# Kernel tuning notes

Hardware: AMD Instinct MI355X
Metric: run time of the kernel (lower is better)

The kernel has to match this reference:

```python
import jax, jax.numpy as jnp
import numpy as np
from jax.ops import segment_sum, segment_max

NEG_SLOPE = 0.2  # PyG GATv2Conv default

def _gatv2(x, ei, ea, Wl, bl, Wr, br, We, att, b, n):
    # PyG GATv2Conv, heads=1, concat=True, add_self_loops=True, fill_value='mean'
    src, dst = ei[0], ei[1]
    ones = jnp.ones((src.shape[0],), x.dtype)
    deg = segment_sum(ones, dst, num_segments=n)
    ea_mean = segment_sum(ea, dst, num_segments=n) / jnp.maximum(deg, 1.0)[:, None]
    loop = jnp.arange(n, dtype=src.dtype)
    src = jnp.concatenate([src, loop]); dst = jnp.concatenate([dst, loop])
    ea = jnp.concatenate([ea, ea_mean], axis=0)
    xl = x @ Wl.T + bl          # lin_l, used for both message and source term
    xr = x @ Wr.T + br          # lin_r, target term
    h = jax.nn.leaky_relu(xl[src] + xr[dst] + ea @ We.T, NEG_SLOPE)  # [E+N, F]
    logits = h @ att            # [E+N]
    m = segment_max(logits, dst, num_segments=n)   # every node has a self-loop -> finite
    p = jnp.exp(logits - m[dst])
    denom = segment_sum(p, dst, num_segments=n)
    alpha = p / denom[dst]
    return segment_sum(alpha[:, None] * xl[src], dst, num_segments=n) + b

def _mean_pool(h, seg, num):
    s = segment_sum(h, seg, num_segments=num)
    c = segment_sum(jnp.ones(h.shape[:1], h.dtype), seg, num_segments=num)
    return s / jnp.maximum(c, 1.0)[:, None]

def setup_inputs() -> dict:
    key = jax.random.key(0)
    ks = iter(jax.random.split(key, 64))
    def nrm(shape, scale=None):
        s = scale if scale is not None else 1.0 / np.sqrt(shape[-1])
        return jax.random.normal(next(ks), shape, jnp.float32) * s
    N, E = 80000, 1280000
    NR, ER, R = 20480, 40960, 512
    inp = {
        'x': nrm((N, 16), 1.0),
        'edge_attr': nrm((E, 18), 1.0),
        'rule_x': nrm((NR, 16), 1.0),
        'rule_edge_attr': nrm((ER, 18), 1.0),
    }
    def gat(fi, fo):
        return (nrm((fo, fi)), jnp.zeros(fo), nrm((fo, fi)), jnp.zeros(fo),
                nrm((fo, 18)), nrm((fo,), 1.0 / np.sqrt(fo)), jnp.zeros(fo))
    for name, (fi, fo) in [('gat0', (16, 100)), ('gat1', (16, 100)), ('gat2', (100, 200))]:
        for suf, v in zip(['Wl', 'bl', 'Wr', 'br', 'We', 'att', 'b'], gat(fi, fo)):
            inp[name + '_' + suf] = v
    inp['lin_W'] = nrm((400, 200)); inp['lin_b'] = jnp.zeros(400)
    inp['f1_W'] = nrm((200, 400)); inp['f1_b'] = jnp.zeros(200)
    inp['f2_W'] = nrm((100, 200)); inp['f2_b'] = jnp.zeros(100)
    inp['f3_W'] = nrm((100, 100)); inp['f3_b'] = jnp.zeros(100)
    inp['bil_W'] = nrm((1, 100, 100)); inp['bil_b'] = jnp.zeros(1)
    inp['edge_index'] = jax.random.randint(next(ks), (2, E), 0, N, dtype=jnp.int32)
    inp['batch'] = jnp.zeros((N,), jnp.int32)
    inp['rule_edge_index'] = jax.random.randint(next(ks), (2, ER), 0, NR, dtype=jnp.int32)
    inp['rule_batch'] = jnp.sort(jax.random.randint(next(ks), (NR,), 0, R, dtype=jnp.int32))
    inp['n_rules'] = R
    return inp

def reference(x, edge_attr, rule_x, rule_edge_attr,
              gat0_Wl, gat0_bl, gat0_Wr, gat0_br, gat0_We, gat0_att, gat0_b,
              gat1_Wl, gat1_bl, gat1_Wr, gat1_br, gat1_We, gat1_att, gat1_b,
              gat2_Wl, gat2_bl, gat2_Wr, gat2_br, gat2_We, gat2_att, gat2_b,
              lin_W, lin_b, f1_W, f1_b, f2_W, f2_b, f3_W, f3_b, bil_W, bil_b,
              edge_index, batch, rule_edge_index, rule_batch, n_rules):
    N = x.shape[0]; NR = rule_x.shape[0]
    # --- RuleParse path ---
    h = jax.nn.relu(_gatv2(rule_x, rule_edge_index, rule_edge_attr,
                           gat1_Wl, gat1_bl, gat1_Wr, gat1_br, gat1_We, gat1_att, gat1_b, NR))
    h = jax.nn.relu(_gatv2(h, rule_edge_index, rule_edge_attr,
                           gat2_Wl, gat2_bl, gat2_Wr, gat2_br, gat2_We, gat2_att, gat2_b, NR))
    h = h @ lin_W.T + lin_b                          # [NR, 400]
    y = _mean_pool(h, rule_batch, n_rules)           # [R, 400]
    y = jax.nn.relu(y @ f1_W.T + f1_b)
    y = jax.nn.relu(y @ f2_W.T + f2_b)
    y = y @ f3_W.T + f3_b                            # [R, 100]
    # --- data path ---
    g = _gatv2(x, edge_index, edge_attr,
               gat0_Wl, gat0_bl, gat0_Wr, gat0_br, gat0_We, gat0_att, gat0_b, N)
    xp = _mean_pool(g, batch, 1)                     # single graph -> [1, 100]
    xr = jnp.tile(xp, (n_rules, 1))                  # x.repeat(len(rules), 1)
    out = jnp.einsum('nd,ode,ne->no', xr, bil_W, y) + bil_b  # Bilinear(100,100,1) -> [R,1]
    return out.T.squeeze()                           # [R]
```

## Files before the change

### kernel.cpp

```cpp
#include <hip/hip_runtime.h>

#define NS 0.2f

__global__ void k_deg(const int* __restrict__ dst, int* degi, int E){
  int stride = gridDim.x * blockDim.x;
  for(int e = blockIdx.x * blockDim.x + threadIdx.x; e < E; e += stride)
    atomicAdd(&degi[dst[e]], 1);
}

__device__ __forceinline__ int wave_iscan(int v, int lane){
  #pragma unroll
  for(int o = 1; o < 64; o <<= 1){
    int t = __shfl_up(v, o);
    if(lane >= o) v += t;
  }
  return v;
}

__global__ __launch_bounds__(1024) void k_scan_sum(
    const int* __restrict__ deg, int* __restrict__ bsum, int n)
{
  __shared__ int wsum[16];
  const int lane = threadIdx.x & 63;
  const int w = threadIdx.x >> 6;
  int idx = blockIdx.x * 1024 + threadIdx.x;
  int v = (idx < n) ? deg[idx] : 0;
  #pragma unroll
  for(int o = 32; o; o >>= 1) v += __shfl_xor(v, o);
  if(lane == 0) wsum[w] = v;
  __syncthreads();
  if(w == 0){
    int s = (lane < 16) ? wsum[lane] : 0;
    #pragma unroll
// ... 22 lines not shown
    const int* __restrict__ deg, const int* __restrict__ bsum,
    int* __restrict__ rowoff, int* __restrict__ pos, int n)
{
  __shared__ int wsum[16];
  const int lane = threadIdx.x & 63;
  const int w = threadIdx.x >> 6;
  int idx = blockIdx.x * 1024 + threadIdx.x;
  int v = (idx < n) ? deg[idx] : 0;
  int inc = wave_iscan(v, lane);
  if(lane == 63) wsum[w] = inc;
  __syncthreads();
  if(w == 0){
    int s = (lane < 16) ? wsum[lane] : 0;
    s = wave_iscan(s, lane);
    if(lane < 16) wsum[lane] = s;
  }
  __syncthreads();
  int woff = (w > 0) ? wsum[w - 1] : 0;
  if(idx < n){
    int ex = bsum[blockIdx.x] + woff + inc - v;
    rowoff[idx] = ex;
    pos[idx] = ex;
  }
}

__global__ void k_fill(const int* __restrict__ dst, int* pos, int* eidx, int E){
  int stride = gridDim.x * blockDim.x;
  for(int e = blockIdx.x * blockDim.x + threadIdx.x; e < E; e += stride){
    int slot = atomicAdd(&pos[dst[e]], 1);
    eidx[slot] = e;
  }
}

__global__ __launch_bounds__(256) void k_easum(
    const float* __restrict__ ea, const int* __restrict__ rowoff,
    const int* __restrict__ eidx, float* __restrict__ eam, int n)
{
  const int lane = threadIdx.x & 63;
  const int wid  = threadIdx.x >> 6;
  const int i = blockIdx.x * 4 + wid;
  if(i >= n) return;
  const int r0 = rowoff[i], r1 = rowoff[i + 1];
  const int deg = r1 - r0;
  const int pg = lane / 18;
  const int k  = lane - pg * 18;
  float s = 0.0f;
  if(pg < 3){
    for(int p = r0 + pg; p < r1; p += 3)
      s += ea[(long)eidx[p] * 18 + k];
  }
  float b = __shfl(s, lane + 18);
  float c = __shfl(s, lane + 36);
  if(lane < 18) eam[(long)i * 18 + lane] = (s + b + c) / fmaxf((float)deg, 1.0f);
}

#define BM 64
#define BN 64
#define BK 16
__global__ __launch_bounds__(256) void k_gemm(
    const float* __restrict__ A, const float* __restrict__ W,
    const float* __restrict__ b, float* __restrict__ C,
    int n, int K, int M, int dorelu)
{
  __shared__ float As[BK][BM + 4];
  __shared__ float Bs[BK][BN + 4];
  const int bi = blockIdx.x * BM;
  const int bj = blockIdx.y * BN;
  const int tid = threadIdx.x;
  const int tr = tid / 16, tc = tid % 16;
  float acc[4][4] = {};
  for(int k0 = 0; k0 < K; k0 += BK){
    for(int l = tid; l < BM * BK; l += 256){
      int c = l % BK, r = l / BK;
      int gr = bi + r, gc = k0 + c;
      As[c][r] = (gr < n && gc < K) ? A[(long)gr * K + gc] : 0.0f;
    }
    for(int l = tid; l < BN * BK; l += 256){
      int c = l % BK, r = l / BK;
      int gr = bj + r, gc = k0 + c;
      Bs[c][r] = (gr < M && gc < K) ? W[(long)gr * K + gc] : 0.0f;
    }
    __syncthreads();
    #pragma unroll
    for(int kk = 0; kk < BK; ++kk){
      float4 av = *(const float4*)&As[kk][tr * 4];
      float4 bv = *(const float4*)&Bs[kk][tc * 4];
      acc[0][0] = fmaf(av.x, bv.x, acc[0][0]); acc[0][1] = fmaf(av.x, bv.y, acc[0][1]);
      acc[0][2] = fmaf(av.x, bv.z, acc[0][2]); acc[0][3] = fmaf(av.x, bv.w, acc[0][3]);
      acc[1][0] = fmaf(av.y, bv.x, acc[1][0]); acc[1][1] = fmaf(av.y, bv.y, acc[1][1]);
      acc[1][2] = fmaf(av.y, bv.z, acc[1][2]); acc[1][3] = fmaf(av.y, bv.w, acc[1][3]);
      acc[2][0] = fmaf(av.z, bv.x, acc[2][0]); acc[2][1] = fmaf(av.z, bv.y, acc[2][1]);
      acc[2][2] = fmaf(av.z, bv.z, acc[2][2]); acc[2][3] = fmaf(av.z, bv.w, acc[2][3]);
      acc[3][0] = fmaf(av.w, bv.x, acc[3][0]); acc[3][1] = fmaf(av.w, bv.y, acc[3][1]);
      acc[3][2] = fmaf(av.w, bv.z, acc[3][2]); acc[3][3] = fmaf(av.w, bv.w, acc[3][3]);
    }
    __syncthreads();
  }
  for(int r = 0; r < 4; r++){
    int gr = bi + tr * 4 + r;
    if(gr >= n) continue;
    for(int c = 0; c < 4; c++){
      int gc = bj + tc * 4 + c;
      if(gc >= M) continue;
      float val = acc[r][c] + b[gc];
      C[(long)gr * M + gc] = dorelu ? fmaxf(val, 0.0f) : val;
    }
  }
}

static void gemm_launch(const float* A, const float* W, const float* b, float* C,
                        int n, int K, int M, int relu, hipStream_t s){
  dim3 grid((n + BM - 1) / BM, (M + BN - 1) / BN);
  k_gemm<<<grid, 256, 0, s>>>(A, W, b, C, n, K, M, relu);
}

__device__ __forceinline__ float lkrelu(float t){ return (t > 0.0f) ? t : NS * t; }

template<int G, int F>
__global__ __launch_bounds__(256) void k_edge_logits(
    const float* __restrict__ xl, const float* __restrict__ xr,
    const float* __restrict__ ea,
    const int* __restrict__ src, const int* __restrict__ dst,
    const int* __restrict__ eidx,
    const float* __restrict__ We, const float* __restrict__ att,
    float2* __restrict__ lw, int E)
{
  constexpr int NG = 256 / G;
  constexpr int NE = 4;
  constexpr int FQ = F / 4;
  __shared__ float4 sWeT[18 * FQ];
  __shared__ float4 sAtt[FQ];
  __shared__ float4 sEa[NG][18];
  __shared__ int    sIdx[NG][3][NE];

  const int tid = threadIdx.x;
  for(int idx = tid; idx < F * 18; idx += 256){
    int f = idx / 18, k = idx % 18;
    ((float*)sWeT)[k * F + f] = We[idx];
  }
  for(int f = tid; f < F; f += 256) ((float*)sAtt)[f] = att[f];
  __syncthreads();

  const int g  = tid / G;
  const int gl = tid % G;
  const bool act = (gl * 4 < F);
  const int glc = act ? gl : 0;
  const long step = (long)gridDim.x * (NG * NE);

  for(long base = (long)blockIdx.x * (NG * NE); base < (long)E; base += step){
    const long pb = base + (long)g * NE;
    if(gl < NE){
      long p = pb + gl;
      int e = -1, s = 0, d = 0;
      if(p < (long)E){ e = eidx[p]; s = src[e]; d = dst[e]; }
      sIdx[g][0][gl] = e; sIdx[g][1][gl] = s; sIdx[g][2][gl] = d;
    }
    #pragma unroll
    for(int t = 0; t < (9 * NE + G - 1) / G; ++t){
      int u = t * G + gl;
      if(u < 9 * NE){
        int ne = u & 3, k2 = u >> 2;
        int e = sIdx[g][0][ne];
        float2 v = (e >= 0) ? *(const float2*)(ea + (long)e * 18 + k2 * 2)
                            : make_float2(0.0f, 0.0f);
        ((float*)&sEa[g][k2 * 2 + 0])[ne] = v.x;
        ((float*)&sEa[g][k2 * 2 + 1])[ne] = v.y;
      }
    }
    int4 sv = *(const int4*)&sIdx[g][1][0];
    int4 dv = *(const int4*)&sIdx[g][2][0];
    float4 a0 = *(const float4*)(xl + (long)sv.x * F + glc * 4);
    float4 b0 = *(const float4*)(xr + (long)dv.x * F + glc * 4);
    float4 a1 = *(const float4*)(xl + (long)sv.y * F + glc * 4);
    float4 b1 = *(const float4*)(xr + (long)dv.y * F + glc * 4);
    float4 a2 = *(const float4*)(xl + (long)sv.z * F + glc * 4);
    float4 b2 = *(const float4*)(xr + (long)dv.z * F + glc * 4);
    float4 a3 = *(const float4*)(xl + (long)sv.w * F + glc * 4);
    float4 b3 = *(const float4*)(xr + (long)dv.w * F + glc * 4);
    float4 t0 = make_float4(a0.x + b0.x, a0.y + b0.y, a0.z + b0.z, a0.w + b0.w);
    float4 t1 = make_float4(a1.x + b1.x, a1.y + b1.y, a1.z + b1.z, a1.w + b1.w);
    float4 t2 = make_float4(a2.x + b2.x, a2.y + b2.y, a2.z + b2.z, a2.w + b2.w);
    float4 t3 = make_float4(a3.x + b3.x, a3.y + b3.y, a3.z + b3.z, a3.w + b3.w);
    #pragma unroll
    for(int k = 0; k < 18; ++k){
      float4 w  = sWeT[k * FQ + glc];
      float4 eq = sEa[g][k];
      t0.x = fmaf(w.x, eq.x, t0.x); t0.y = fmaf(w.y, eq.x, t0.y);
      t0.z = fmaf(w.z, eq.x, t0.z); t0.w = fmaf(w.w, eq.x, t0.w);
      t1.x = fmaf(w.x, eq.y, t1.x); t1.y = fmaf(w.y, eq.y, t1.y);
      t1.z = fmaf(w.z, eq.y, t1.z); t1.w = fmaf(w.w, eq.y, t1.w);
      t2.x = fmaf(w.x, eq.z, t2.x); t2.y = fmaf(w.y, eq.z, t2.y);
      t2.z = fmaf(w.z, eq.z, t2.z); t2.w = fmaf(w.w, eq.z, t2.w);
      t3.x = fmaf(w.x, eq.w, t3.x); t3.y = fmaf(w.y, eq.w, t3.y);
      t3.z = fmaf(w.z, eq.w, t3.z); t3.w = fmaf(w.w, eq.w, t3.w);
    }
    float4 av = sAtt[glc];
    float r0 = 0, r1 = 0, r2 = 0, r3 = 0;
    if(act){
      r0 = av.x * lkrelu(t0.x) + av.y * lkrelu(t0.y) + av.z * lkrelu(t0.z) + av.w * lkrelu(t0.w);
      r1 = av.x * lkrelu(t1.x) + av.y * lkrelu(t1.y) + av.z * lkrelu(t1.z) + av.w * lkrelu(t1.w);
      r2 = av.x * lkrelu(t2.x) + av.y * lkrelu(t2.y) + av.z * lkrelu(t2.z) + av.w * lkrelu(t2.w);
      r3 = av.x * lkrelu(t3.x) + av.y * lkrelu(t3.y) + av.z * lkrelu(t3.z) + av.w * lkrelu(t3.w);
    }
    #pragma unroll
    for(int o = G / 2; o; o >>= 1){
      r0 += __shfl_xor(r0, o);
      r1 += __shfl_xor(r1, o);
      r2 += __shfl_xor(r2, o);
      r3 += __shfl_xor(r3, o);
    }
    if(gl == 0 && pb + 0 < (long)E) lw[pb + 0] = make_float2(r0, __int_as_float(sv.x));
    if(gl == 1 && pb + 1 < (long)E) lw[pb + 1] = make_float2(r1, __int_as_float(sv.y));
    if(gl == 2 && pb + 2 < (long)E) lw[pb + 2] = make_float2(r2, __int_as_float(sv.z));
    if(gl == 3 && pb + 3 < (long)E) lw[pb + 3] = make_float2(r3, __int_as_float(sv.w));
  }
}

#define CH 128
template<int JMAX>
__global__ __launch_bounds__(256) void k_gat_agg(
    const float* __restrict__ xl, const float* __restrict__ xr,
    const float* __restrict__ eam,
    const float* __restrict__ We, const float* __restrict__ att,
    const int* __restrict__ rowoff, const float2* __restrict__ lw,
    const float* __restrict__ bias, float* __restrict__ out,
    int n, int F, int dorelu)
{
  const int lane = threadIdx.x & 63;
  const int wid  = threadIdx.x >> 6;
  __shared__ float2 s_ws[4][CH];
  const int i = blockIdx.x * 4 + wid;
  if(i >= n) return;
  const int r0 = rowoff[i], r1 = rowoff[i + 1];
  const int deg = r1 - r0;

  float eamv[18];
  #pragma unroll
  for(int k = 0; k < 18; ++k) eamv[k] = eam[(long)i * 18 + k];

  float selfl = 0.0f;
  float acc[JMAX];
  #pragma unroll
  for(int j = 0; j < JMAX; ++j){
    int f = lane + j * 64;
    float xv = (f < F) ? xl[(long)i * F + f] : 0.0f;
    acc[j] = xv;
    if(f < F){
      float t = xv + xr[(long)i * F + f];
      const float* w = We + f * 18;
      #pragma unroll
      for(int k = 0; k < 18; ++k) t = fmaf(w[k], eamv[k], t);
      t = lkrelu(t);
      selfl = fmaf(att[f], t, selfl);
    }
  }
  #pragma unroll
  for(int o = 32; o; o >>= 1) selfl += __shfl_xor(selfl, o);

  float m = selfl, denom = 1.0f;

  for(int c0 = 0; c0 < deg; c0 += CH){
    int cn = min(CH, deg - c0);
    float lmax = -3.4e38f;
    for(int q = lane; q < cn; q += 64){
      float2 ws = lw[r0 + c0 + q];
      s_ws[wid][q] = ws;
      lmax = fmaxf(lmax, ws.x);
    }
    #pragma unroll
    for(int o = 32; o; o >>= 1) lmax = fmaxf(lmax, __shfl_xor(lmax, o));
    float newm = fmaxf(m, lmax);
    float scale = __expf(m - newm);
    denom *= scale;
    #pragma unroll
    for(int j = 0; j < JMAX; ++j) acc[j] *= scale;
    m = newm;
    float psum = 0.0f;
    for(int q = lane; q < cn; q += 64){
      float2 ws = s_ws[wid][q];
      float w = __expf(ws.x - m);
      s_ws[wid][q].x = w;
      psum += w;
    }
    #pragma unroll
    for(int o = 32; o; o >>= 1) psum += __shfl_xor(psum, o);
    denom += psum;
    int p = 0;
    for(; p + 8 <= cn; p += 8){
      float2 wv[8];
      const float* xs[8];
      #pragma unroll
      for(int u = 0; u < 8; ++u){
        wv[u] = s_ws[wid][p + u];
        xs[u] = xl + (long)__float_as_int(wv[u].y) * F;
      }
      float vv[8][JMAX];
      #pragma unroll
      for(int u = 0; u < 8; ++u)
        #pragma unroll
        for(int j = 0; j < JMAX; ++j){
          int f = lane + j * 64;
          vv[u][j] = (f < F) ? xs[u][f] : 0.0f;
        }
      #pragma unroll
      for(int u = 0; u < 8; ++u)
        #pragma unroll
        for(int j = 0; j < JMAX; ++j)
          acc[j] = fmaf(wv[u].x, vv[u][j], acc[j]);
    }
    for(; p < cn; ++p){
      float2 ws = s_ws[wid][p];
      const float* xs = xl + (long)__float_as_int(ws.y) * F;
      #pragma unroll
      for(int j = 0; j < JMAX; ++j){
        int f = lane + j * 64;
        if(f < F) acc[j] = fmaf(ws.x, xs[f], acc[j]);
      }
    }
  }

  float inv = 1.0f / denom;
  #pragma unroll
  for(int j = 0; j < JMAX; ++j){
    int f = lane + j * 64;
    if(f < F){
      float o = acc[j] * inv + bias[f];
      out[(long)i * F + f] = dorelu ? fmaxf(o, 0.0f) : o;
    }
  }
}

__global__ void k_rule_starts(const int* __restrict__ rb, int* starts, int NR, int R){
  int r = blockIdx.x * blockDim.x + threadIdx.x;
  if(r > R) return;
  if(r == R){ starts[R] = NR; return; }
  int lo = 0, hi = NR;
  while(lo < hi){ int mid = (lo + hi) >> 1; if(rb[mid] < r) lo = mid + 1; else hi = mid; }
  starts[r] = lo;
}

__global__ void k_pool_rules(const float* __restrict__ h, const int* __restrict__ starts,
                             float* __restrict__ y, int R, int F){
  long idx = (long)blockIdx.x * blockDim.x + threadIdx.x;
  long total = (long)R * F;
  if(idx >= total) return;
  int r = (int)(idx / F);
  int f = (int)(idx % F);
  int s0 = starts[r], s1 = starts[r + 1];
  float a = 0.0f;
  for(int i = s0; i < s1; i++) a += h[(long)i * F + f];
  y[idx] = a / fmaxf((float)(s1 - s0), 1.0f);
}

__global__ __launch_bounds__(256) void k_pool_all(
    const float* __restrict__ g, float* xp, int n, int F)
{
  const int lane = threadIdx.x & 63;
  const int wid  = threadIdx.x >> 6;
  const int nw   = 4;
  float a0 = 0.0f, a1 = 0.0f;
// ... 15 lines not shown
  }
}

__global__ __launch_bounds__(512) void k_bil(
    const float* __restrict__ xp, const float* __restrict__ Wb,
    const float* __restrict__ y, const float* __restrict__ bilb,
    float* __restrict__ out, float inv_n, int R)
{
  __shared__ float v[100];
  int t = threadIdx.x;
  if(t < 100){
    float a = 0.0f;
    for(int d = 0; d < 100; d++) a += xp[d] * Wb[d * 100 + t];
    v[t] = a * inv_n;
  }
  __syncthreads();
  for(int r = t; r < R; r += 512){
    float a = 0.0f;
    const float* yr = y + (long)r * 100;
    for(int e = 0; e < 100; e++) a += v[e] * yr[e];
    out[r] = a + bilb[0];
  }
}

static inline int nblk(long n){
  long b = (n + 255) / 256;
  if(b > 20480) b = 20480;
  if(b < 1) b = 1;
  return (int)b;
}

struct GatParams { const float *Wl,*bl,*Wr,*br,*We,*att,*b; };

template<int G, int F>
static void logits_launch(const float* xl, const float* xr, const float* ea,
                          const int* src, const int* dst, const int* eidx,
                          const float* We, const float* att, float2* lw,
                          int E, hipStream_t stream){
  const int epb = (256 / G) * 4;
  long nb = ((long)E + epb - 1) / epb;
  int grid = (int)(nb < 2048 ? nb : 2048);
  k_edge_logits<G, F><<<grid, 256, 0, stream>>>(xl, xr, ea, src, dst, eidx, We, att, lw, E);
}

static void scan_launch(const int* degi, int* bsum, int* rowoff, int* pos,
                        int n, hipStream_t stream){
  int B = (n + 1023) / 1024;
  k_scan_sum  <<<B, 1024, 0, stream>>>(degi, bsum, n);
  k_scan_bsum <<<1, 128,  0, stream>>>(bsum, rowoff, B, n);
  k_scan_apply<<<B, 1024, 0, stream>>>(degi, bsum, rowoff, pos, n);
}

static void run_gatv2(const float* x, int fin, int fout, int n,
                      const int* src, const int* dst, const float* ea, int E,
                      GatParams P, float* out, int dorelu,
                      float* xl, float* xr, float2* lw,
                      const float* eam, const int* rowoff, const int* eidx,
                      hipStream_t stream){
  gemm_launch(x, P.Wl, P.bl, xl, n, fin, fout, 0, stream);
  gemm_launch(x, P.Wr, P.br, xr, n, fin, fout, 0, stream);
  if(fout == 100){
    logits_launch<32, 100>(xl, xr, ea, src, dst, eidx, P.We, P.att, lw, E, stream);
    k_gat_agg<2><<<(n + 3) / 4, 256, 0, stream>>>(xl, xr, eam, P.We, P.att,
                                                  rowoff, lw, P.b, out, n, fout, dorelu);
  } else {
    logits_launch<64, 200>(xl, xr, ea, src, dst, eidx, P.We, P.att, lw, E, stream);
    k_gat_agg<4><<<(n + 3) / 4, 256, 0, stream>>>(xl, xr, eam, P.We, P.att,
                                                  rowoff, lw, P.b, out, n, fout, dorelu);
  }
}

extern "C" void kernel_launch(void* const* d_in, const int* in_sizes, int n_in,
                              void* d_out, int out_size, void* d_ws, size_t ws_size,
                              hipStream_t stream){
  const float* x   = (const float*)d_in[0];
  const float* ea  = (const float*)d_in[1];
  const float* rx  = (const float*)d_in[2];
  const float* rea = (const float*)d_in[3];
  GatParams g0{ (const float*)d_in[4],  (const float*)d_in[5],  (const float*)d_in[6],
                (const float*)d_in[7],  (const float*)d_in[8],  (const float*)d_in[9],
                (const float*)d_in[10] };
  GatParams g1{ (const float*)d_in[11], (const float*)d_in[12], (const float*)d_in[13],
                (const float*)d_in[14], (const float*)d_in[15], (const float*)d_in[16],
                (const float*)d_in[17] };
  GatParams g2{ (const float*)d_in[18], (const float*)d_in[19], (const float*)d_in[20],
                (const float*)d_in[21], (const float*)d_in[22], (const float*)d_in[23],
                (const float*)d_in[24] };
  const float* lin_W = (const float*)d_in[25]; const float* lin_b = (const float*)d_in[26];
  const float* f1_W  = (const float*)d_in[27]; const float* f1_b  = (const float*)d_in[28];
  const float* f2_W  = (const float*)d_in[29]; const float* f2_b  = (const float*)d_in[30];
  const float* f3_W  = (const float*)d_in[31]; const float* f3_b  = (const float*)d_in[32];
  const float* bilW  = (const float*)d_in[33]; const float* bilb  = (const float*)d_in[34];
  const int* ei  = (const int*)d_in[35];
  const int* rei = (const int*)d_in[37];
  const int* rb  = (const int*)d_in[38];

  const int N  = in_sizes[0] / 16;
  const int E  = in_sizes[1] / 18;
  const int NR = in_sizes[2] / 16;
  const int ER = in_sizes[3] / 18;
  const int R  = out_size;

  float* Wf = (float*)d_ws;
  size_t off = 0;
  auto alloc  = [&](size_t nf){ nf = (nf + 1) & ~(size_t)1; float* p = Wf + off; off += nf; return p; };
  auto alloci = [&](size_t ni){ ni = (ni + 1) & ~(size_t)1; int* p = (int*)(Wf + off); off += ni; return p; };

  float* y0 = alloc((size_t)R * 400);
  float* y1 = alloc((size_t)R * 200);
  float* y2 = alloc((size_t)R * 100);
  float* y3 = alloc((size_t)R * 100);
  float* xp = alloc(128);
  int* starts = alloci(R + 1);
  const size_t arena = off;

  {
    off = arena;
    float* h1 = alloc((size_t)NR * 100);
    float* h2 = alloc((size_t)NR * 200);
    float* xl = alloc((size_t)NR * 200);
    float* xr = alloc((size_t)NR * 200);
    float2* lw = (float2*)alloc((size_t)ER * 2);
    float* eam   = alloc((size_t)NR * 18);
    int* rowoff = alloci(NR + 1);
    int* degi   = alloci(NR);
    int* pos    = alloci(NR);
    int* bsum   = alloci(128);
    int* eidx   = alloci(ER);
    const int* rsrc = rei; const int* rdst = rei + ER;

    hipMemsetAsync(degi, 0, (size_t)NR * 4, stream);
    k_deg<<<nblk(ER), 256, 0, stream>>>(rdst, degi, ER);
    scan_launch(degi, bsum, rowoff, pos, NR, stream);
    k_fill<<<nblk(ER), 256, 0, stream>>>(rdst, pos, eidx, ER);
    k_easum<<<(NR + 3) / 4, 256, 0, stream>>>(rea, rowoff, eidx, eam, NR);

    run_gatv2(rx, 16, 100, NR, rsrc, rdst, rea, ER, g1, h1, 1,
              xl, xr, lw, eam, rowoff, eidx, stream);
    run_gatv2(h1, 100, 200, NR, rsrc, rdst, rea, ER, g2, h2, 1,
              xl, xr, lw, eam, rowoff, eidx, stream);

    float* hlin = xl;
    gemm_launch(h2, lin_W, lin_b, hlin, NR, 200, 400, 0, stream);

    k_rule_starts<<<(R + 256) / 256, 256, 0, stream>>>(rb, starts, NR, R);
    k_pool_rules<<<nblk((long)R * 400), 256, 0, stream>>>(hlin, starts, y0, R, 400);

    gemm_launch(y0, f1_W, f1_b, y1, R, 400, 200, 1, stream);
    gemm_launch(y1, f2_W, f2_b, y2, R, 200, 100, 1, stream);
    gemm_launch(y2, f3_W, f3_b, y3, R, 100, 100, 0, stream);
  }

  {
    off = arena;
    float* g  = alloc((size_t)N * 100);
    float* xl = alloc((size_t)N * 100);
    float* xr = alloc((size_t)N * 100);
    float2* lw = (float2*)alloc((size_t)E * 2);
    float* eam   = alloc((size_t)N * 18);
    int* rowoff = alloci((size_t)N + 1);
    int* degi   = alloci(N);
    int* pos    = alloci(N);
    int* bsum   = alloci(128);
    int* eidx   = alloci(E);
    const int* srcp = ei; const int* dstp = ei + E;

    hipMemsetAsync(degi, 0, (size_t)N * 4, stream);
    k_deg<<<nblk(E), 256, 0, stream>>>(dstp, degi, E);
    scan_launch(degi, bsum, rowoff, pos, N, stream);
    k_fill<<<nblk(E), 256, 0, stream>>>(dstp, pos, eidx, E);
    k_easum<<<(N + 3) / 4, 256, 0, stream>>>(ea, rowoff, eidx, eam, N);

    run_gatv2(x, 16, 100, N, srcp, dstp, ea, E, g0, g, 0,
              xl, xr, lw, eam, rowoff, eidx, stream);

    hipMemsetAsync(xp, 0, 128 * 4, stream);
    k_pool_all<<<1024, 256, 0, stream>>>(g, xp, N, 100);
    k_bil<<<1, 512, 0, stream>>>(xp, bilW, y3, bilb, (float*)d_out, 1.0f / (float)N, R);
  }
}
```

Baseline: 1.032 ms.

## Fuse GATv2 edge logits, self-loop mean, and aggregation into one CSR kernel; fp16 xl/xr

Replaces the separate edge-logit kernel, edge-attr mean kernel and aggregation kernel with one node-centric kernel. It walks each destination's CSR edge list, computes logits, runs an online softmax and accumulates messages in a single pass. The mean edge attribute is built on the fly for the self-loop term. For the large data graph, the xl/xr projections are stored in fp16 to halve gather traffic. This removes the intermediate logit buffer and extra passes, at the cost of fp16 rounding and possible load imbalance on high-degree nodes.

```diff
diff --git a/kernel.cpp b/kernel.cpp
--- a/kernel.cpp
+++ b/kernel.cpp
@@ -1,4 +1,5 @@
 #include <hip/hip_runtime.h>
+#include <hip/hip_fp16.h>
 
 #define NS 0.2f
 
@@ -87,28 +88,6 @@
   }
 }
 
-__global__ __launch_bounds__(256) void k_easum(
-    const float* __restrict__ ea, const int* __restrict__ rowoff,
-    const int* __restrict__ eidx, float* __restrict__ eam, int n)
-{
-  const int lane = threadIdx.x & 63;
-  const int wid  = threadIdx.x >> 6;
-  const int i = blockIdx.x * 4 + wid;
-  if(i >= n) return;
-  const int r0 = rowoff[i], r1 = rowoff[i + 1];
-  const int deg = r1 - r0;
-  const int pg = lane / 18;
-  const int k  = lane - pg * 18;
-  float s = 0.0f;
-  if(pg < 3){
-    for(int p = r0 + pg; p < r1; p += 3)
-      s += ea[(long)eidx[p] * 18 + k];
-  }
-  float b = __shfl(s, lane + 18);
-  float c = __shfl(s, lane + 36);
-  if(lane < 18) eam[(long)i * 18 + lane] = (s + b + c) / fmaxf((float)deg, 1.0f);
-}
-
 #define BM 64
 #define BN 64
 #define BK 16
@@ -163,30 +142,98 @@
   }
 }
 
+__global__ __launch_bounds__(256) void k_gemm_h(
+    const float* __restrict__ A, const float* __restrict__ W,
+    const float* __restrict__ b, __half* __restrict__ C,
+    int n, int K, int M)
+{
+  __shared__ float As[BK][BM + 4];
+  __shared__ float Bs[BK][BN + 4];
+  const int bi = blockIdx.x * BM;
+  const int bj = blockIdx.y * BN;
+  const int tid = threadIdx.x;
+  const int tr = tid / 16, tc = tid % 16;
+  float acc[4][4] = {};
+  for(int k0 = 0; k0 < K; k0 += BK){
+    for(int l = tid; l < BM * BK; l += 256){
+      int c = l % BK, r = l / BK;
+      int gr = bi + r, gc = k0 + c;
+      As[c][r] = (gr < n && gc < K) ? A[(long)gr * K + gc] : 0.0f;
+    }
+    for(int l = tid; l < BN * BK; l += 256){
+      int c = l % BK, r = l / BK;
+      int gr = bj + r, gc = k0 + c;
+      Bs[c][r] = (gr < M && gc < K) ? W[(long)gr * K + gc] : 0.0f;
+    }
+    __syncthreads();
+    #pragma unroll
+    for(int kk = 0; kk < BK; ++kk){
+      float4 av = *(const float4*)&As[kk][tr * 4];
+      float4 bv = *(const float4*)&Bs[kk][tc * 4];
+      acc[0][0] = fmaf(av.x, bv.x, acc[0][0]); acc[0][1] = fmaf(av.x, bv.y, acc[0][1]);
+      acc[0][2] = fmaf(av.x, bv.z, acc[0][2]); acc[0][3] = fmaf(av.x, bv.w, acc[0][3]);
+      acc[1][0] = fmaf(av.y, bv.x, acc[1][0]); acc[1][1] = fmaf(av.y, bv.y, acc[1][1]);
+      acc[1][2] = fmaf(av.y, bv.z, acc[1][2]); acc[1][3] = fmaf(av.y, bv.w, acc[1][3]);
+      acc[2][0] = fmaf(av.z, bv.x, acc[2][0]); acc[2][1] = fmaf(av.z, bv.y, acc[2][1]);
+      acc[2][2] = fmaf(av.z, bv.z, acc[2][2]); acc[2][3] = fmaf(av.z, bv.w, acc[2][3]);
+      acc[3][0] = fmaf(av.w, bv.x, acc[3][0]); acc[3][1] = fmaf(av.w, bv.y, acc[3][1]);
+      acc[3][2] = fmaf(av.w, bv.z, acc[3][2]); acc[3][3] = fmaf(av.w, bv.w, acc[3][3]);
+    }
+    __syncthreads();
+  }
+  for(int r = 0; r < 4; r++){
+    int gr = bi + tr * 4 + r;
+    if(gr >= n) continue;
+    int gc0 = bj + tc * 4;
+    float v[4];
+    #pragma unroll
+    for(int c = 0; c < 4; c++){
+      int gc = gc0 + c;
+      v[c] = (gc < M) ? acc[r][c] + b[gc] : 0.0f;
+    }
+    __half* Crow = C + (long)gr * M;
+    if(gc0 + 3 < M){
+      *(__half2*)(Crow + gc0)     = __halves2half2(__float2half(v[0]), __float2half(v[1]));
+      *(__half2*)(Crow + gc0 + 2) = __halves2half2(__float2half(v[2]), __float2half(v[3]));
+    } else {
+      for(int c = 0; c < 4; c++){
+        int gc = gc0 + c;
+        if(gc < M) Crow[gc] = __float2half(v[c]);
+      }
+    }
+  }
+}
+
 static void gemm_launch(const float* A, const float* W, const float* b, float* C,
                         int n, int K, int M, int relu, hipStream_t s){
   dim3 grid((n + BM - 1) / BM, (M + BN - 1) / BN);
   k_gemm<<<grid, 256, 0, s>>>(A, W, b, C, n, K, M, relu);
 }
 
+static void gemm_h_launch(const float* A, const float* W, const float* b, __half* C,
+                          int n, int K, int M, hipStream_t s){
+  dim3 grid((n + BM - 1) / BM, (M + BN - 1) / BN);
+  k_gemm_h<<<grid, 256, 0, s>>>(A, W, b, C, n, K, M);
+}
+
 __device__ __forceinline__ float lkrelu(float t){ return (t > 0.0f) ? t : NS * t; }
 
 template<int G, int F>
-__global__ __launch_bounds__(256) void k_edge_logits(
+__global__ __launch_bounds__(256) void k_gat_fused(
     const float* __restrict__ xl, const float* __restrict__ xr,
-    const float* __restrict__ ea,
-    const int* __restrict__ src, const int* __restrict__ dst,
-    const int* __restrict__ eidx,
+    const float* __restrict__ ea, const int* __restrict__ src,
+    const int* __restrict__ rowoff, const int* __restrict__ eidx,
     const float* __restrict__ We, const float* __restrict__ att,
-    float2* __restrict__ lw, int E)
+    const float* __restrict__ bias, float* __restrict__ out,
+    int n, int dorelu)
 {
   constexpr int NG = 256 / G;
-  constexpr int NE = 4;
   constexpr int FQ = F / 4;
   __shared__ float4 sWeT[18 * FQ];
   __shared__ float4 sAtt[FQ];
   __shared__ float4 sEa[NG][18];
-  __shared__ int    sIdx[NG][3][NE];
+  __shared__ float  sEamAcc[NG][18];
+  __shared__ int    sIdx[NG][2][4];
 
   const int tid = threadIdx.x;
   for(int idx = tid; idx < F * 18; idx += 256){
@@ -196,191 +243,279 @@
   for(int f = tid; f < F; f += 256) ((float*)sAtt)[f] = att[f];
   __syncthreads();
 
-  const int g  = tid / G;
-  const int gl = tid % G;
+  const int g = tid / G, gl = tid % G;
   const bool act = (gl * 4 < F);
   const int glc = act ? gl : 0;
-  const long step = (long)gridDim.x * (NG * NE);
-
-  for(long base = (long)blockIdx.x * (NG * NE); base < (long)E; base += step){
-    const long pb = base + (long)g * NE;
-    if(gl < NE){
-      long p = pb + gl;
-      int e = -1, s = 0, d = 0;
-      if(p < (long)E){ e = eidx[p]; s = src[e]; d = dst[e]; }
-      sIdx[g][0][gl] = e; sIdx[g][1][gl] = s; sIdx[g][2][gl] = d;
-    }
-    #pragma unroll
-    for(int t = 0; t < (9 * NE + G - 1) / G; ++t){
-      int u = t * G + gl;
-      if(u < 9 * NE){
-        int ne = u & 3, k2 = u >> 2;
-        int e = sIdx[g][0][ne];
-        float2 v = (e >= 0) ? *(const float2*)(ea + (long)e * 18 + k2 * 2)
-                            : make_float2(0.0f, 0.0f);
-        ((float*)&sEa[g][k2 * 2 + 0])[ne] = v.x;
-        ((float*)&sEa[g][k2 * 2 + 1])[ne] = v.y;
-      }
-    }
-    int4 sv = *(const int4*)&sIdx[g][1][0];
-    int4 dv = *(const int4*)&sIdx[g][2][0];
-    float4 a0 = *(const float4*)(xl + (long)sv.x * F + glc * 4);
-    float4 b0 = *(const float4*)(xr + (long)dv.x * F + glc * 4);
-    float4 a1 = *(const float4*)(xl + (long)sv.y * F + glc * 4);
-    float4 b1 = *(const float4*)(xr + (long)dv.y * F + glc * 4);
-    float4 a2 = *(const float4*)(xl + (long)sv.z * F + glc * 4);
-    float4 b2 = *(const float4*)(xr + (long)dv.z * F + glc * 4);
-    float4 a3 = *(const float4*)(xl + (long)sv.w * F + glc * 4);
-    float4 b3 = *(const float4*)(xr + (long)dv.w * F + glc * 4);
-    float4 t0 = make_float4(a0.x + b0.x, a0.y + b0.y, a0.z + b0.z, a0.w + b0.w);
-    float4 t1 = make_float4(a1.x + b1.x, a1.y + b1.y, a1.z + b1.z, a1.w + b1.w);
-    float4 t2 = make_float4(a2.x + b2.x, a2.y + b2.y, a2.z + b2.z, a2.w + b2.w);
-    float4 t3 = make_float4(a3.x + b3.x, a3.y + b3.y, a3.z + b3.z, a3.w + b3.w);
+  const float4 av = sAtt[glc];
+
+  for(int node = blockIdx.x * NG + g; node < n; node += gridDim.x * NG){
+    const int r0 = rowoff[node], r1 = rowoff[node + 1];
+    const int deg = r1 - r0;
+    if(gl < 18) sEamAcc[g][gl] = 0.0f;
+    float4 xlv = *(const float4*)(xl + (long)node * F + glc * 4);
+    float4 xrv = *(const float4*)(xr + (long)node * F + glc * 4);
+    float m = -3.4e38f, denom = 0.0f;
+    float4 acc = make_float4(0.f, 0.f, 0.f, 0.f);
+
+    for(int p = r0; p < r1; p += 4){
+      if(gl < 4){
+        int pp = p + gl; int e = -1, s = 0;
+        if(pp < r1){ e = eidx[pp]; s = src[e]; }
+        sIdx[g][0][gl] = e; sIdx[g][1][gl] = s;
+      }
+      #pragma unroll
+      for(int t = 0; t < (36 + G - 1) / G; ++t){
+        int u = t * G + gl;
+        if(u < 36){
+          int ne = u & 3, k2 = u >> 2;
+          int e = sIdx[g][0][ne];
+          float2 v = (e >= 0) ? *(const float2*)(ea + (long)e * 18 + k2 * 2)
+                              : make_float2(0.f, 0.f);
+          ((float*)&sEa[g][k2 * 2 + 0])[ne] = v.x;
+          ((float*)&sEa[g][k2 * 2 + 1])[ne] = v.y;
+        }
+      }
+      int4 sv = *(const int4*)&sIdx[g][1][0];
+      if(gl < 18){ float4 eq = sEa[g][gl]; sEamAcc[g][gl] += eq.x + eq.y + eq.z + eq.w; }
+      float4 a0 = *(const float4*)(xl + (long)sv.x * F + glc * 4);
+      float4 a1 = *(const float4*)(xl + (long)sv.y * F + glc * 4);
+      float4 a2 = *(const float4*)(xl + (long)sv.z * F + glc * 4);
+      float4 a3 = *(const float4*)(xl + (long)sv.w * F + glc * 4);
+      float4 t0 = make_float4(a0.x + xrv.x, a0.y + xrv.y, a0.z + xrv.z, a0.w + xrv.w);
+      float4 t1 = make_float4(a1.x + xrv.x, a1.y + xrv.y, a1.z + xrv.z, a1.w + xrv.w);
+      float4 t2 = make_float4(a2.x + xrv.x, a2.y + xrv.y, a2.z + xrv.z, a2.w + xrv.w);
+      float4 t3 = make_float4(a3.x + xrv.x, a3.y + xrv.y, a3.z + xrv.z, a3.w + xrv.w);
+      #pragma unroll
+      for(int k = 0; k < 18; ++k){
+        float4 w  = sWeT[k * FQ + glc];
+        float4 eq = sEa[g][k];
+        t0.x = fmaf(w.x, eq.x, t0.x); t0.y = fmaf(w.y, eq.x, t0.y);
+        t0.z = fmaf(w.z, eq.x, t0.z); t0.w = fmaf(w.w, eq.x, t0.w);
+        t1.x = fmaf(w.x, eq.y, t1.x); t1.y = fmaf(w.y, eq.y, t1.y);
+        t1.z = fmaf(w.z, eq.y, t1.z); t1.w = fmaf(w.w, eq.y, t1.w);
+        t2.x = fmaf(w.x, eq.z, t2.x); t2.y = fmaf(w.y, eq.z, t2.y);
+        t2.z = fmaf(w.z, eq.z, t2.z); t2.w = fmaf(w.w, eq.z, t2.w);
+        t3.x = fmaf(w.x, eq.w, t3.x); t3.y = fmaf(w.y, eq.w, t3.y);
+        t3.z = fmaf(w.z, eq.w, t3.z); t3.w = fmaf(w.w, eq.w, t3.w);
+      }
+      float l0 = 0, l1 = 0, l2 = 0, l3 = 0;
+      if(act){
+        l0 = av.x * lkrelu(t0.x) + av.y * lkrelu(t0.y) + av.z * lkrelu(t0.z) + av.w * lkrelu(t0.w);
+        l1 = av.x * lkrelu(t1.x) + av.y * lkrelu(t1.y) + av.z * lkrelu(t1.z) + av.w * lkrelu(t1.w);
+        l2 = av.x * lkrelu(t2.x) + av.y * lkrelu(t2.y) + av.z * lkrelu(t2.z) + av.w * lkrelu(t2.w);
+        l3 = av.x * lkrelu(t3.x) + av.y * lkrelu(t3.y) + av.z * lkrelu(t3.z) + av.w * lkrelu(t3.w);
+      }
+      #pragma unroll
+      for(int o = G / 2; o; o >>= 1){
+        l0 += __shfl_xor(l0, o);
+        l1 += __shfl_xor(l1, o);
+        l2 += __shfl_xor(l2, o);
+        l3 += __shfl_xor(l3, o);
+      }
+      bool v1 = (p + 1 < r1), v2 = (p + 2 < r1), v3 = (p + 3 < r1);
+      if(!v1) l1 = -3.4e38f;
+      if(!v2) l2 = -3.4e38f;
+      if(!v3) l3 = -3.4e38f;
+      float bmax = fmaxf(fmaxf(l0, l1), fmaxf(l2, l3));
+      float newm = fmaxf(m, bmax);
+      float sc = __expf(m - newm);
+      denom *= sc;
+      acc.x *= sc; acc.y *= sc; acc.z *= sc; acc.w *= sc;
+      m = newm;
+      float w0 = __expf(l0 - m);
+      float w1 = v1 ? __expf(l1 - m) : 0.0f;
+      float w2 = v2 ? __expf(l2 - m) : 0.0f;
+      float w3 = v3 ? __expf(l3 - m) : 0.0f;
+      denom += w0 + w1 + w2 + w3;
+      acc.x += w0 * a0.x + w1 * a1.x + w2 * a2.x + w3 * a3.x;
+      acc.y += w0 * a0.y + w1 * a1.y + w2 * a2.y + w3 * a3.y;
+      acc.z += w0 * a0.z + w1 * a1.z + w2 * a2.z + w3 * a3.z;
+      acc.w += w0 * a0.w + w1 * a1.w + w2 * a2.w + w3 * a3.w;
+    }
+
+    float inv_deg = 1.0f / fmaxf((float)deg, 1.0f);
+    float4 ts = make_float4(xlv.x + xrv.x, xlv.y + xrv.y, xlv.z + xrv.z, xlv.w + xrv.w);
     #pragma unroll
     for(int k = 0; k < 18; ++k){
-      float4 w  = sWeT[k * FQ + glc];
-      float4 eq = sEa[g][k];
-      t0.x = fmaf(w.x, eq.x, t0.x); t0.y = fmaf(w.y, eq.x, t0.y);
-      t0.z = fmaf(w.z, eq.x, t0.z); t0.w = fmaf(w.w, eq.x, t0.w);
-      t1.x = fmaf(w.x, eq.y, t1.x); t1.y = fmaf(w.y, eq.y, t1.y);
-      t1.z = fmaf(w.z, eq.y, t1.z); t1.w = fmaf(w.w, eq.y, t1.w);
-      t2.x = fmaf(w.x, eq.z, t2.x); t2.y = fmaf(w.y, eq.z, t2.y);
-      t2.z = fmaf(w.z, eq.z, t2.z); t2.w = fmaf(w.w, eq.z, t2.w);
-      t3.x = fmaf(w.x, eq.w, t3.x); t3.y = fmaf(w.y, eq.w, t3.y);
-      t3.z = fmaf(w.z, eq.w, t3.z); t3.w = fmaf(w.w, eq.w, t3.w);
-    }
-    float4 av = sAtt[glc];
-    float r0 = 0, r1 = 0, r2 = 0, r3 = 0;
+      float em = sEamAcc[g][k] * inv_deg;
+      float4 w = sWeT[k * FQ + glc];
+      ts.x = fmaf(w.x, em, ts.x); ts.y = fmaf(w.y, em, ts.y);
+      ts.z = fmaf(w.z, em, ts.z); ts.w = fmaf(w.w, em, ts.w);
+    }
+    float sl = 0.0f;
+    if(act) sl = av.x * lkrelu(ts.x) + av.y * lkrelu(ts.y) + av.z * lkrelu(ts.z) + av.w * lkrelu(ts.w);
+    #pragma unroll
+    for(int o = G / 2; o; o >>= 1) sl += __shfl_xor(sl, o);
+    float newm = fmaxf(m, sl);
+    float sc = __expf(m - newm);
+    float ws = __expf(sl - newm);
+    denom = denom * sc + ws;
+    acc.x = acc.x * sc + ws * xlv.x;
+    acc.y = acc.y * sc + ws * xlv.y;
+    acc.z = acc.z * sc + ws * xlv.z;
+    acc.w = acc.w * sc + ws * xlv.w;
+
     if(act){
-      r0 = av.x * lkrelu(t0.x) + av.y * lkrelu(t0.y) + av.z * lkrelu(t0.z) + av.w * lkrelu(t0.w);
-      r1 = av.x * lkrelu(t1.x) + av.y * lkrelu(t1.y) + av.z * lkrelu(t1.z) + av.w * lkrelu(t1.w);
-      r2 = av.x * lkrelu(t2.x) + av.y * lkrelu(t2.y) + av.z * lkrelu(t2.z) + av.w * lkrelu(t2.w);
-      r3 = av.x * lkrelu(t3.x) + av.y * lkrelu(t3.y) + av.z * lkrelu(t3.z) + av.w * lkrelu(t3.w);
-    }
+      float inv = 1.0f / denom;
+      float4 bv = *(const float4*)(bias + glc * 4);
+      float4 ov = make_float4(acc.x * inv + bv.x, acc.y * inv + bv.y,
+                              acc.z * inv + bv.z, acc.w * inv + bv.w);
+      if(dorelu){
+        ov.x = fmaxf(ov.x, 0.f); ov.y = fmaxf(ov.y, 0.f);
+        ov.z = fmaxf(ov.z, 0.f); ov.w = fmaxf(ov.w, 0.f);
+      }
+      *(float4*)(out + (long)node * F + glc * 4) = ov;
+    }
+  }
+}
+
+__global__ __launch_bounds__(256) void k_gat_fused_h(
+    const __half* __restrict__ xl, const __half* __restrict__ xr,
+    const float* __restrict__ ea, const int* __restrict__ src,
+    const int* __restrict__ rowoff, const int* __restrict__ eidx,
+    const float* __restrict__ We, const float* __restrict__ att,
+    const float* __restrict__ bias, float* __restrict__ out, int n)
+{
+  constexpr int G = 32, NG = 8, F = 100, FQ = 25;
+  __shared__ float4 sWeT[18 * FQ];
+  __shared__ float4 sAtt[FQ];
+  __shared__ float4 sEa[NG][18];
+  __shared__ float  sEamAcc[NG][18];
+  __shared__ int    sIdx[NG][2][4];
+
+  const int tid = threadIdx.x;
+  for(int idx = tid; idx < F * 18; idx += 256){
+    int f = idx / 18, k = idx % 18;
+    ((float*)sWeT)[k * F + f] = We[idx];
+  }
+  for(int f = tid; f < F; f += 256) ((float*)sAtt)[f] = att[f];
+  __syncthreads();
+
+  const int g = tid / G, gl = tid % G;
+  const bool act = (gl * 4 < F);
+  const int glc = act ? gl : 0;
+  const float4 av = sAtt[glc];
+
+  auto ld4h = [&](const __half* bp, long row) -> float4 {
+    uint2 u = *(const uint2*)(bp + row * F + glc * 4);
+    float2 lo = __half22float2(*(__half2*)&u.x);
+    float2 hi = __half22float2(*(__half2*)&u.y);
+    return make_float4(lo.x, lo.y, hi.x, hi.y);
+  };
+
+  for(int node = blockIdx.x * NG + g; node < n; node += gridDim.x * NG){
+    const int r0 = rowoff[node], r1 = rowoff[node + 1];
+    const int deg = r1 - r0;
+    if(gl < 18) sEamAcc[g][gl] = 0.0f;
+    float4 xlv = ld4h(xl, node);
+    float4 xrv = ld4h(xr, node);
+    float m = -3.4e38f, denom = 0.0f;
+    float4 acc = make_float4(0.f, 0.f, 0.f, 0.f);
+
+    for(int p = r0; p < r1; p += 4){
+      if(gl < 4){
+        int pp = p + gl; int e = -1, s = 0;
+        if(pp < r1){ e = eidx[pp]; s = src[e]; }
+        sIdx[g][0][gl] = e; sIdx[g][1][gl] = s;
+      }
+      #pragma unroll
+      for(int t = 0; t < 2; ++t){
+        int u = t * G + gl;
+        if(u < 36){
+          int ne = u & 3, k2 = u >> 2;
+          int e = sIdx[g][0][ne];
+          float2 v = (e >= 0) ? *(const float2*)(ea + (long)e * 18 + k2 * 2)
+                              : make_float2(0.f, 0.f);
+          ((float*)&sEa[g][k2 * 2 + 0])[ne] = v.x;
+          ((float*)&sEa[g][k2 * 2 + 1])[ne] = v.y;
+        }
+      }
+      int4 sv = *(const int4*)&sIdx[g][1][0];
+      if(gl < 18){ float4 eq = sEa[g][gl]; sEamAcc[g][gl] += eq.x + eq.y + eq.z + eq.w; }
+      float4 a0 = ld4h(xl, sv.x);
+      float4 a1 = ld4h(xl, sv.y);
+      float4 a2 = ld4h(xl, sv.z);
+      float4 a3 = ld4h(xl, sv.w);
+      float4 t0 = make_float4(a0.x + xrv.x, a0.y + xrv.y, a0.z + xrv.z, a0.w + xrv.w);
+      float4 t1 = make_float4(a1.x + xrv.x, a1.y + xrv.y, a1.z + xrv.z, a1.w + xrv.w);
+      float4 t2 = make_float4(a2.x + xrv.x, a2.y + xrv.y, a2.z + xrv.z, a2.w + xrv.w);
+      float4 t3 = make_float4(a3.x + xrv.x, a3.y + xrv.y, a3.z + xrv.z, a3.w + xrv.w);
+      #pragma unroll
+      for(int k = 0; k < 18; ++k){
+        float4 w  = sWeT[k * FQ + glc];
+        float4 eq = sEa[g][k];
+        t0.x = fmaf(w.x, eq.x, t0.x); t0.y = fmaf(w.y, eq.x, t0.y);
+        t0.z = fmaf(w.z, eq.x, t0.z); t0.w = fmaf(w.w, eq.x, t0.w);
+        t1.x = fmaf(w.x, eq.y, t1.x); t1.y = fmaf(w.y, eq.y, t1.y);
+        t1.z = fmaf(w.z, eq.y, t1.z); t1.w = fmaf(w.w, eq.y, t1.w);
+        t2.x = fmaf(w.x, eq.z, t2.x); t2.y = fmaf(w.y, eq.z, t2.y);
+        t2.z = fmaf(w.z, eq.z, t2.z); t2.w = fmaf(w.w, eq.z, t2.w);
+        t3.x = fmaf(w.x, eq.w, t3.x); t3.y = fmaf(w.y, eq.w, t3.y);
+        t3.z = fmaf(w.z, eq.w, t3.z); t3.w = fmaf(w.w, eq.w, t3.w);
+      }
+      float l0 = 0, l1 = 0, l2 = 0, l3 = 0;
+      if(act){
+        l0 = av.x * lkrelu(t0.x) + av.y * lkrelu(t0.y) + av.z * lkrelu(t0.z) + av.w * lkrelu(t0.w);
+        l1 = av.x * lkrelu(t1.x) + av.y * lkrelu(t1.y) + av.z * lkrelu(t1.z) + av.w * lkrelu(t1.w);
+        l2 = av.x * lkrelu(t2.x) + av.y * lkrelu(t2.y) + av.z * lkrelu(t2.z) + av.w * lkrelu(t2.w);
+        l3 = av.x * lkrelu(t3.x) + av.y * lkrelu(t3.y) + av.z * lkrelu(t3.z) + av.w * lkrelu(t3.w);
+      }
+      #pragma unroll
+      for(int o = G / 2; o; o >>= 1){
+        l0 += __shfl_xor(l0, o);
+        l1 += __shfl_xor(l1, o);
+        l2 += __shfl_xor(l2, o);
+        l3 += __shfl_xor(l3, o);
+      }
+      bool v1 = (p + 1 < r1), v2 = (p + 2 < r1), v3 = (p + 3 < r1);
+      if(!v1) l1 = -3.4e38f;
+      if(!v2) l2 = -3.4e38f;
+      if(!v3) l3 = -3.4e38f;
+      float bmax = fmaxf(fmaxf(l0, l1), fmaxf(l2, l3));
+      float newm = fmaxf(m, bmax);
+      float sc = __expf(m - newm);
+      denom *= sc;
+      acc.x *= sc; acc.y *= sc; acc.z *= sc; acc.w *= sc;
+      m = newm;
+      float w0 = __expf(l0 - m);
+      float w1 = v1 ? __expf(l1 - m) : 0.0f;
+      float w2 = v2 ? __expf(l2 - m) : 0.0f;
+      float w3 = v3 ? __expf(l3 - m) : 0.0f;
+      denom += w0 + w1 + w2 + w3;
+      acc.x += w0 * a0.x + w1 * a1.x + w2 * a2.x + w3 * a3.x;
+      acc.y += w0 * a0.y + w1 * a1.y + w2 * a2.y + w3 * a3.y;
+      acc.z += w0 * a0.z + w1 * a1.z + w2 * a2.z + w3 * a3.z;
+      acc.w += w0 * a0.w + w1 * a1.w + w2 * a2.w + w3 * a3.w;
+    }
+
+    float inv_deg = 1.0f / fmaxf((float)deg, 1.0f);
+    float4 ts = make_float4(xlv.x + xrv.x, xlv.y + xrv.y, xlv.z + xrv.z, xlv.w + xrv.w);
     #pragma unroll
-    for(int o = G / 2; o; o >>= 1){
-      r0 += __shfl_xor(r0, o);
-      r1 += __shfl_xor(r1, o);
-      r2 += __shfl_xor(r2, o);
-      r3 += __shfl_xor(r3, o);
-    }
-    if(gl == 0 && pb + 0 < (long)E) lw[pb + 0] = make_float2(r0, __int_as_float(sv.x));
-    if(gl == 1 && pb + 1 < (long)E) lw[pb + 1] = make_float2(r1, __int_as_float(sv.y));
-    if(gl == 2 && pb + 2 < (long)E) lw[pb + 2] = make_float2(r2, __int_as_float(sv.z));
-    if(gl == 3 && pb + 3 < (long)E) lw[pb + 3] = make_float2(r3, __int_as_float(sv.w));
-  }
-}
-
-#define CH 128
-template<int JMAX>
-__global__ __launch_bounds__(256) void k_gat_agg(
-    const float* __restrict__ xl, const float* __restrict__ xr,
-    const float* __restrict__ eam,
-    const float* __restrict__ We, const float* __restrict__ att,
-    const int* __restrict__ rowoff, const float2* __restrict__ lw,
-    const float* __restrict__ bias, float* __restrict__ out,
-    int n, int F, int dorelu)
-{
-  const int lane = threadIdx.x & 63;
-  const int wid  = threadIdx.x >> 6;
-  __shared__ float2 s_ws[4][CH];
-  const int i = blockIdx.x * 4 + wid;
-  if(i >= n) return;
-  const int r0 = rowoff[i], r1 = rowoff[i + 1];
-  const int deg = r1 - r0;
-
-  float eamv[18];
-  #pragma unroll
-  for(int k = 0; k < 18; ++k) eamv[k] = eam[(long)i * 18 + k];
-
-  float selfl = 0.0f;
-  float acc[JMAX];
-  #pragma unroll
-  for(int j = 0; j < JMAX; ++j){
-    int f = lane + j * 64;
-    float xv = (f < F) ? xl[(long)i * F + f] : 0.0f;
-    acc[j] = xv;
-    if(f < F){
-      float t = xv + xr[(long)i * F + f];
-      const float* w = We + f * 18;
-      #pragma unroll
-      for(int k = 0; k < 18; ++k) t = fmaf(w[k], eamv[k], t);
-      t = lkrelu(t);
-      selfl = fmaf(att[f], t, selfl);
-    }
-  }
-  #pragma unroll
-  for(int o = 32; o; o >>= 1) selfl += __shfl_xor(selfl, o);
-
-  float m = selfl, denom = 1.0f;
-
-  for(int c0 = 0; c0 < deg; c0 += CH){
-    int cn = min(CH, deg - c0);
-    float lmax = -3.4e38f;
-    for(int q = lane; q < cn; q += 64){
-      float2 ws = lw[r0 + c0 + q];
-      s_ws[wid][q] = ws;
-      lmax = fmaxf(lmax, ws.x);
-    }
+    for(int k = 0; k < 18; ++k){
+      float em = sEamAcc[g][k] * inv_deg;
+      float4 w = sWeT[k * FQ + glc];
+      ts.x = fmaf(w.x, em, ts.x); ts.y = fmaf(w.y, em, ts.y);
+      ts.z = fmaf(w.z, em, ts.z); ts.w = fmaf(w.w, em, ts.w);
+    }
+    float sl = 0.0f;
+    if(act) sl = av.x * lkrelu(ts.x) + av.y * lkrelu(ts.y) + av.z * lkrelu(ts.z) + av.w * lkrelu(ts.w);
     #pragma unroll
-    for(int o = 32; o; o >>= 1) lmax = fmaxf(lmax, __shfl_xor(lmax, o));
-    float newm = fmaxf(m, lmax);
-    float scale = __expf(m - newm);
-    denom *= scale;
-    #pragma unroll
-    for(int j = 0; j < JMAX; ++j) acc[j] *= scale;
-    m = newm;
-    float psum = 0.0f;
-    for(int q = lane; q < cn; q += 64){
-      float2 ws = s_ws[wid][q];
-      float w = __expf(ws.x - m);
-      s_ws[wid][q].x = w;
-      psum += w;
-    }
-    #pragma unroll
-    for(int o = 32; o; o >>= 1) psum += __shfl_xor(psum, o);
-    denom += psum;
-    int p = 0;
-    for(; p + 8 <= cn; p += 8){
-      float2 wv[8];
-      const float* xs[8];
-      #pragma unroll
-      for(int u = 0; u < 8; ++u){
-        wv[u] = s_ws[wid][p + u];
-        xs[u] = xl + (long)__float_as_int(wv[u].y) * F;
-      }
-      float vv[8][JMAX];
-      #pragma unroll
-      for(int u = 0; u < 8; ++u)
-        #pragma unroll
-        for(int j = 0; j < JMAX; ++j){
-          int f = lane + j * 64;
-          vv[u][j] = (f < F) ? xs[u][f] : 0.0f;
-        }
-      #pragma unroll
-      for(int u = 0; u < 8; ++u)
-        #pragma unroll
-        for(int j = 0; j < JMAX; ++j)
-          acc[j] = fmaf(wv[u].x, vv[u][j], acc[j]);
-    }
-    for(; p < cn; ++p){
-      float2 ws = s_ws[wid][p];
-      const float* xs = xl + (long)__float_as_int(ws.y) * F;
-      #pragma unroll
-      for(int j = 0; j < JMAX; ++j){
-        int f = lane + j * 64;
-        if(f < F) acc[j] = fmaf(ws.x, xs[f], acc[j]);
-      }
-    }
-  }
-
-  float inv = 1.0f / denom;
-  #pragma unroll
-  for(int j = 0; j < JMAX; ++j){
-    int f = lane + j * 64;
-    if(f < F){
-      float o = acc[j] * inv + bias[f];
-      out[(long)i * F + f] = dorelu ? fmaxf(o, 0.0f) : o;
+    for(int o = G / 2; o; o >>= 1) sl += __shfl_xor(sl, o);
+    float newm = fmaxf(m, sl);
+    float sc = __expf(m - newm);
+    float ws = __expf(sl - newm);
+    denom = denom * sc + ws;
+    acc.x = acc.x * sc + ws * xlv.x;
+    acc.y = acc.y * sc + ws * xlv.y;
+    acc.z = acc.z * sc + ws * xlv.z;
+    acc.w = acc.w * sc + ws * xlv.w;
+
+    if(act){
+      float inv = 1.0f / denom;
+      float4 bv = *(const float4*)(bias + glc * 4);
+      float4 ov = make_float4(acc.x * inv + bv.x, acc.y * inv + bv.y,
+                              acc.z * inv + bv.z, acc.w * inv + bv.w);
+      *(float4*)(out + (long)node * F + glc * 4) = ov;
     }
   }
 }
@@ -462,17 +597,6 @@
 
 struct GatParams { const float *Wl,*bl,*Wr,*br,*We,*att,*b; };
 
-template<int G, int F>
-static void logits_launch(const float* xl, const float* xr, const float* ea,
-                          const int* src, const int* dst, const int* eidx,
-                          const float* We, const float* att, float2* lw,
-                          int E, hipStream_t stream){
-  const int epb = (256 / G) * 4;
-  long nb = ((long)E + epb - 1) / epb;
-  int grid = (int)(nb < 2048 ? nb : 2048);
-  k_edge_logits<G, F><<<grid, 256, 0, stream>>>(xl, xr, ea, src, dst, eidx, We, att, lw, E);
-}
-
 static void scan_launch(const int* degi, int* bsum, int* rowoff, int* pos,
                         int n, hipStream_t stream){
   int B = (n + 1023) / 1024;
@@ -481,23 +605,31 @@
   k_scan_apply<<<B, 1024, 0, stream>>>(degi, bsum, rowoff, pos, n);
 }
 
+template<int G, int F>
+static void gat_fused_launch(const float* xl, const float* xr, const float* ea,
+                             const int* src, const int* rowoff, const int* eidx,
+                             const float* We, const float* att, const float* bias,
+                             float* out, int n, int dorelu, hipStream_t stream){
+  constexpr int NG = 256 / G;
+  long nb = ((long)n + NG - 1) / NG;
+  int grid = (int)(nb < 4096 ? nb : 4096);
+  k_gat_fused<G, F><<<grid, 256, 0, stream>>>(xl, xr, ea, src, rowoff, eidx,
+                                              We, att, bias, out, n, dorelu);
+}
+
 static void run_gatv2(const float* x, int fin, int fout, int n,
-                      const int* src, const int* dst, const float* ea, int E,
+                      const int* src, const float* ea,
                       GatParams P, float* out, int dorelu,
-                      float* xl, float* xr, float2* lw,
-                      const float* eam, const int* rowoff, const int* eidx,
-                      hipStream_t stream){
+                      float* xl, float* xr,
+                      const int* rowoff, const int* eidx, hipStream_t stream){
   gemm_launch(x, P.Wl, P.bl, xl, n, fin, fout, 0, stream);
   gemm_launch(x, P.Wr, P.br, xr, n, fin, fout, 0, stream);
-  if(fout == 100){
-    logits_launch<32, 100>(xl, xr, ea, src, dst, eidx, P.We, P.att, lw, E, stream);
-    k_gat_agg<2><<<(n + 3) / 4, 256, 0, stream>>>(xl, xr, eam, P.We, P.att,
-                                                  rowoff, lw, P.b, out, n, fout, dorelu);
-  } else {
-    logits_launch<64, 200>(xl, xr, ea, src, dst, eidx, P.We, P.att, lw, E, stream);
-    k_gat_agg<4><<<(n + 3) / 4, 256, 0, stream>>>(xl, xr, eam, P.We, P.att,
-                                                  rowoff, lw, P.b, out, n, fout, dorelu);
-  }
+  if(fout == 100)
+    gat_fused_launch<32, 100>(xl, xr, ea, src, rowoff, eidx, P.We, P.att, P.b,
+                              out, n, dorelu, stream);
+  else
+    gat_fused_launch<64, 200>(xl, xr, ea, src, rowoff, eidx, P.We, P.att, P.b,
+                              out, n, dorelu, stream);
 }
 
 extern "C" void kernel_launch(void* const* d_in, const int* in_sizes, int n_in,
@@ -550,8 +682,6 @@
     float* h2 = alloc((size_t)NR * 200);
     float* xl = alloc((size_t)NR * 200);
     float* xr = alloc((size_t)NR * 200);
-    float2* lw = (float2*)alloc((size_t)ER * 2);
-    float* eam   = alloc((size_t)NR * 18);
     int* rowoff = alloci(NR + 1);
     int* degi   = alloci(NR);
     int* pos    = alloci(NR);
@@ -563,12 +693,9 @@
     k_deg<<<nblk(ER), 256, 0, stream>>>(rdst, degi, ER);
     scan_launch(degi, bsum, rowoff, pos, NR, stream);
     k_fill<<<nblk(ER), 256, 0, stream>>>(rdst, pos, eidx, ER);
-    k_easum<<<(NR + 3) / 4, 256, 0, stream>>>(rea, rowoff, eidx, eam, NR);
-
-    run_gatv2(rx, 16, 100, NR, rsrc, rdst, rea, ER, g1, h1, 1,
-              xl, xr, lw, eam, rowoff, eidx, stream);
-    run_gatv2(h1, 100, 200, NR, rsrc, rdst, rea, ER, g2, h2, 1,
-              xl, xr, lw, eam, rowoff, eidx, stream);
+
+    run_gatv2(rx, 16, 100, NR, rsrc, rea, g1, h1, 1, xl, xr, rowoff, eidx, stream);
+    run_gatv2(h1, 100, 200, NR, rsrc, rea, g2, h2, 1, xl, xr, rowoff, eidx, stream);
 
     float* hlin = xl;
     gemm_launch(h2, lin_W, lin_b, hlin, NR, 200, 400, 0, stream);
@@ -584,10 +711,8 @@
   {
     off = arena;
     float* g  = alloc((size_t)N * 100);
-    float* xl = alloc((size_t)N * 100);
-    float* xr = alloc((size_t)N * 100);
-    float2* lw = (float2*)alloc((size_t)E * 2);
-    float* eam   = alloc((size_t)N * 18);
+    __half* xlh = (__half*)alloc((size_t)N * 50);
+    __half* xrh = (__half*)alloc((size_t)N * 50);
     int* rowoff = alloci((size_t)N + 1);
     int* degi   = alloci(N);
     int* pos    = alloci(N);
@@ -599,10 +724,15 @@
     k_deg<<<nblk(E), 256, 0, stream>>>(dstp, degi, E);
     scan_launch(degi, bsum, rowoff, pos, N, stream);
     k_fill<<<nblk(E), 256, 0, stream>>>(dstp, pos, eidx, E);
-    k_easum<<<(N + 3) / 4, 256, 0, stream>>>(ea, rowoff, eidx, eam, N);
-
-    run_gatv2(x, 16, 100, N, srcp, dstp, ea, E, g0, g, 0,
-              xl, xr, lw, eam, rowoff, eidx, stream);
+
+    gemm_h_launch(x, g0.Wl, g0.bl, xlh, N, 16, 100, stream);
+    gemm_h_launch(x, g0.Wr, g0.br, xrh, N, 16, 100, stream);
+    {
+      long nb = ((long)N + 7) / 8;
+      int grid = (int)(nb < 4096 ? nb : 4096);
+      k_gat_fused_h<<<grid, 256, 0, stream>>>(xlh, xrh, ea, srcp, rowoff, eidx,
+                                              g0.We, g0.att, g0.b, g, N);
+    }
 
     hipMemsetAsync(xp, 0, 128 * 4, stream);
     k_pool_all<<<1024, 256, 0, stream>>>(g, xp, N, 100);
```

Result: faster. 886.3 us (-14.1%).
